# Kernel tuning notes

Hardware: AMD Instinct MI355X
Metric: run time of the kernel (lower is better)

Reference implementation:

```python
import jax, jax.numpy as jnp
import numpy as np

NG = 128          # grid points per axis
FEAT = 16         # feature size
WIDTH = 64        # mlp hidden width
OUT = 1
NPTS = 262144
NUM_POS = 3       # sinusoidal frequencies
IN_MLP = FEAT + NUM_POS * 3


def setup_inputs() -> dict:
    key = jax.random.key(0)
    k1, k2, k3, k4, k5, k6 = jax.random.split(key, 6)
    x = jax.random.uniform(k1, (NPTS, 3), dtype=jnp.float32)
    grid = jax.random.normal(k2, (NG, NG, NG, FEAT), dtype=jnp.float32)
    lim1 = 1.0 / np.sqrt(IN_MLP)
    lim2 = 1.0 / np.sqrt(WIDTH)
    w1 = jax.random.uniform(k3, (WIDTH, IN_MLP), minval=-lim1, maxval=lim1, dtype=jnp.float32)
    b1 = jax.random.uniform(k4, (WIDTH,), minval=-lim1, maxval=lim1, dtype=jnp.float32)
    w2 = jax.random.uniform(k5, (OUT, WIDTH), minval=-lim2, maxval=lim2, dtype=jnp.float32)
    b2 = jax.random.uniform(k6, (OUT,), minval=-lim2, maxval=lim2, dtype=jnp.float32)
    return {"x": x, "grid": grid, "w1": w1, "b1": b1, "w2": w2, "b2": b2}


def _cubic_weights(t):
    # Catmull-Rom (a=-0.5) cubic convolution weights over 4-point stencil.
    # t: (..., ) fractional coordinate in [0,1). returns (..., 4)
    t2 = t * t
    t3 = t2 * t
    w0 = 0.5 * (-t3 + 2.0 * t2 - t)
    w1 = 0.5 * (3.0 * t3 - 5.0 * t2 + 2.0)
    w2 = 0.5 * (-3.0 * t3 + 4.0 * t2 + t)
    w3 = 0.5 * (t3 - t2)
    return jnp.stack([w0, w1, w2, w3], axis=-1)


def _forward(x, grid, w1, b1, w2, b2):
    n = grid.shape[0]
    # domain [0,1]^3, uniform spacing h = 1/(n-1); block_frac == fractional cell coord
    u = x * (n - 1.0)                       # (N,3) grid-space coords
    i0 = jnp.floor(u).astype(jnp.int32)
    t = u - i0                              # (N,3) in [0,1)
    offs = jnp.arange(-1, 3, dtype=jnp.int32)
    idx = jnp.clip(i0[:, :, None] + offs, 0, n - 1)   # (N,3,4)
    w = _cubic_weights(t)                   # (N,3,4)
    # 4x4x4 gather per point: (N,4,4,4,F)
    g = grid[idx[:, 0, :, None, None], idx[:, 1, None, :, None], idx[:, 2, None, None, :]]
    feat = jnp.einsum('na,nb,nc,nabcf->nf', w[:, 0], w[:, 1], w[:, 2], g)  # (N,F)
    # sinusoidal pos-encoding: sin(2*pi*k * frac), k=1..3, layout (k, dim) flattened
    mult = 2.0 * jnp.pi * jnp.arange(1, NUM_POS + 1, dtype=x.dtype)        # (3,)
    pos = jnp.sin(mult[None, :, None] * t[:, None, :]).reshape(x.shape[0], -1)  # (N,9)
    h = jnp.concatenate([feat, pos], axis=-1)           # (N, F+9)
    hid = jax.nn.swish(h @ w1.T + b1)                   # (N, WIDTH)
    return hid @ w2.T + b2                              # (N, OUT)


def reference(x, grid, w1, b1, w2, b2):
    return _forward(x, grid, w1, b1, w2, b2)
```

## Files before the change

### kernel.cpp

```cpp
#include <hip/hip_runtime.h>
#include <cmath>

#define NGRID 128
#define FEAT 16
#define WIDTH 64
#define NPTS 262144
#define IN_MLP 25

__device__ __forceinline__ void fma4(float4& a, float w, const float4 c) {
    a.x = fmaf(w, c.x, a.x);
    a.y = fmaf(w, c.y, a.y);
    a.z = fmaf(w, c.z, a.z);
    a.w = fmaf(w, c.w, a.w);
}

__global__ __launch_bounds__(256, 4) void gridnet_kernel(
    const float* __restrict__ x,
    const float* __restrict__ grid,
    const float* __restrict__ w1,
    const float* __restrict__ b1,
    const float* __restrict__ w2,
    const float* __restrict__ b2,
    float* __restrict__ out)
{
    const int p = blockIdx.x * blockDim.x + threadIdx.x;
    if (p >= NPTS) return;

    int   offa[4], offb[4], offc[4];
    float wx[4], wy[4], wz[4];
    float t[3];
    #pragma unroll
    for (int d = 0; d < 3; ++d) {
        const float u  = x[3 * p + d] * 127.0f;
        const float fu = floorf(u);
        const float td = u - fu;
        t[d] = td;
        const int i0 = (int)fu;
        const float t2 = td * td;
        const float t3 = t2 * td;
        float w0 = 0.5f * (-t3 + 2.0f * t2 - td);
        float w1v = 0.5f * (3.0f * t3 - 5.0f * t2 + 2.0f);
        float w2v = 0.5f * (-3.0f * t3 + 4.0f * t2 + td);
        float w3 = 0.5f * (t3 - t2);
        #pragma unroll
        for (int o = 0; o < 4; ++o) {
            int v = i0 - 1 + o;
            v = v < 0 ? 0 : (v > 127 ? 127 : v);
            if (d == 0) offa[o] = v * 65536;
            if (d == 1) offb[o] = v * 512;
            if (d == 2) offc[o] = v * 4;
        }
        float* wp = (d == 0) ? wx : (d == 1) ? wy : wz;
        wp[0] = w0; wp[1] = w1v; wp[2] = w2v; wp[3] = w3;
    }

    float4 acc0 = make_float4(0.f, 0.f, 0.f, 0.f);
    float4 acc1 = acc0, acc2 = acc0, acc3 = acc0;
    const float4* __restrict__ g4 = (const float4*)grid;

    #pragma unroll 1
    for (int a = 0; a < 4; ++a) {
        const float wa = wx[a];
        #pragma unroll 1
        for (int b = 0; b < 4; ++b) {
            const float wab = wa * wy[b];
            const int   rb  = offa[a] + offb[b];
            #pragma unroll
            for (int c = 0; c < 4; ++c) {
                const float w = wab * wz[c];
                const float4* cell = g4 + (rb + offc[c]);
                fma4(acc0, w, cell[0]);
                fma4(acc1, w, cell[1]);
                fma4(acc2, w, cell[2]);
                fma4(acc3, w, cell[3]);
            }
        }
    }

    float h[IN_MLP];
    h[0]  = acc0.x; h[1]  = acc0.y; h[2]  = acc0.z; h[3]  = acc0.w;
    h[4]  = acc1.x; h[5]  = acc1.y; h[6]  = acc1.z; h[7]  = acc1.w;
    h[8]  = acc2.x; h[9]  = acc2.y; h[10] = acc2.z; h[11] = acc2.w;
    h[12] = acc3.x; h[13] = acc3.y; h[14] = acc3.z; h[15] = acc3.w;

    #pragma unroll
    for (int k = 0; k < 3; ++k) {
        #pragma unroll
        for (int d = 0; d < 3; ++d) {
            h[16 + k * 3 + d] = __builtin_amdgcn_sinf((float)(k + 1) * t[d]);
        }
    }

    float o = b2[0];
    #pragma unroll 4
    for (int j = 0; j < WIDTH; ++j) {
        float hj = b1[j];
        #pragma unroll
        for (int k = 0; k < IN_MLP; ++k) {
            hj = fmaf(h[k], w1[j * IN_MLP + k], hj);
        }
        const float sig = 1.0f / (1.0f + __expf(-hj));
        o = fmaf(hj * sig, w2[j], o);
    }
    out[p] = o;
}

extern "C" void kernel_launch(void* const* d_in, const int* in_sizes, int n_in,
                              void* d_out, int out_size, void* d_ws, size_t ws_size,
                              hipStream_t stream) {
    const float* x    = (const float*)d_in[0];
    const float* grid = (const float*)d_in[1];
    const float* w1   = (const float*)d_in[2];
    const float* b1   = (const float*)d_in[3];
    const float* w2   = (const float*)d_in[4];
    const float* b2   = (const float*)d_in[5];
    float* out = (float*)d_out;

    const int threads = 256;
    const int blocks  = (NPTS + threads - 1) / threads;
    gridnet_kernel<<<blocks, threads, 0, stream>>>(x, grid, w1, b1, w2, b2, out);
}
```

Baseline: 689.9 us.

## Sort points into spatial buckets before gathering grid features

Adds a counting sort (histogram, scan, scatter) that groups query points into 8x8x8-cell spatial buckets, then runs the main kernel over the permuted order. An XCD-aware block swizzle is meant to keep neighbouring buckets on the same chiplet's L2. Block size also drops to 128 with a higher occupancy hint. The aim is better cache locality for the random 64-cell gathers from the 128 MB grid. The cost is four extra small launches, atomics, and an indirect perm load per thread.

```diff
diff --git a/kernel.cpp b/kernel.cpp
--- a/kernel.cpp
+++ b/kernel.cpp
@@ -6,6 +6,62 @@
 #define WIDTH 64
 #define NPTS 262144
 #define IN_MLP 25
+#define NB 16
+#define NBUCKETS 4096
+
+#define WS_NEEDED (NBUCKETS * 4 + NPTS * 4)
+
+__device__ __forceinline__ int bucket_of(const float* __restrict__ x, int p) {
+    int key = 0;
+    #pragma unroll
+    for (int d = 0; d < 3; ++d) {
+        int i0 = (int)floorf(x[3 * p + d] * 127.0f);
+        i0 = i0 < 0 ? 0 : (i0 > 126 ? 126 : i0);
+        key = (key << 4) | (i0 >> 3);
+    }
+    return key;
+}
+
+__global__ void zero_hist_kernel(int* __restrict__ hist) {
+    hist[blockIdx.x * 256 + threadIdx.x] = 0;
+}
+
+__global__ void hist_kernel(const float* __restrict__ x, int* __restrict__ hist) {
+    const int p = blockIdx.x * blockDim.x + threadIdx.x;
+    if (p >= NPTS) return;
+    atomicAdd(&hist[bucket_of(x, p)], 1);
+}
+
+__global__ __launch_bounds__(1024) void scan_kernel(int* __restrict__ hist) {
+    __shared__ int lds[1024];
+    const int t = threadIdx.x;
+    int4 v = ((int4*)hist)[t];
+    lds[t] = v.x + v.y + v.z + v.w;
+    __syncthreads();
+    #pragma unroll
+    for (int off = 1; off < 1024; off <<= 1) {
+        int val = lds[t];
+        int add = (t >= off) ? lds[t - off] : 0;
+        __syncthreads();
+        lds[t] = val + add;
+        __syncthreads();
+    }
+    const int excl = (t == 0) ? 0 : lds[t - 1];
+    int4 o;
+    o.x = excl;
+    o.y = excl + v.x;
+    o.z = excl + v.x + v.y;
+    o.w = excl + v.x + v.y + v.z;
+    ((int4*)hist)[t] = o;
+}
+
+__global__ void scatter_kernel(const float* __restrict__ x, int* __restrict__ offs,
+                               int* __restrict__ perm) {
+    const int p = blockIdx.x * blockDim.x + threadIdx.x;
+    if (p >= NPTS) return;
+    const int pos = atomicAdd(&offs[bucket_of(x, p)], 1);
+    perm[pos] = p;
+}
 
 __device__ __forceinline__ void fma4(float4& a, float w, const float4 c) {
     a.x = fmaf(w, c.x, a.x);
@@ -14,17 +70,21 @@
     a.w = fmaf(w, c.w, a.w);
 }
 
-__global__ __launch_bounds__(256, 4) void gridnet_kernel(
+template <bool SORTED>
+__global__ __launch_bounds__(128, 8) void gridnet_kernel(
     const float* __restrict__ x,
     const float* __restrict__ grid,
     const float* __restrict__ w1,
     const float* __restrict__ b1,
     const float* __restrict__ w2,
     const float* __restrict__ b2,
+    const int* __restrict__ perm,
     float* __restrict__ out)
 {
-    const int p = blockIdx.x * blockDim.x + threadIdx.x;
-    if (p >= NPTS) return;
+    const int bid = blockIdx.x;
+    const int swz = SORTED ? ((bid & 7) * 256 + (bid >> 3)) : bid;
+    const int gid = swz * 128 + threadIdx.x;
+    const int p = SORTED ? perm[gid] : gid;
 
     int   offa[4], offb[4], offc[4];
     float wx[4], wy[4], wz[4];
@@ -116,7 +176,17 @@
     const float* b2   = (const float*)d_in[5];
     float* out = (float*)d_out;
 
-    const int threads = 256;
-    const int blocks  = (NPTS + threads - 1) / threads;
-    gridnet_kernel<<<blocks, threads, 0, stream>>>(x, grid, w1, b1, w2, b2, out);
+    if (ws_size >= (size_t)WS_NEEDED) {
+        int* hist = (int*)d_ws;
+        int* perm = (int*)((char*)d_ws + NBUCKETS * 4);
+        zero_hist_kernel<<<NBUCKETS / 256, 256, 0, stream>>>(hist);
+        hist_kernel<<<NPTS / 256, 256, 0, stream>>>(x, hist);
+        scan_kernel<<<1, 1024, 0, stream>>>(hist);
+        scatter_kernel<<<NPTS / 256, 256, 0, stream>>>(x, hist, perm);
+        gridnet_kernel<true><<<NPTS / 128, 128, 0, stream>>>(
+            x, grid, w1, b1, w2, b2, perm, out);
+    } else {
+        gridnet_kernel<false><<<NPTS / 128, 128, 0, stream>>>(
+            x, grid, w1, b1, w2, b2, nullptr, out);
+    }
 }
```

Result: faster. 566.0 us (-18.0%).
